# Kernel tuning notes

Measured on AMD Instinct MI355X. Metric: run time of the kernel, lower is better.

## Reference

```python
import jax, jax.numpy as jnp
import numpy as np
import math

NUM_HEADS = 8
EPS = 1e-5
LEAKY_SLOPE = 0.01


def _attention(q, k, v, mask):
    # q:[S,64] k,v:[T,64] -> [S,64]; scale by sqrt(d) per source (q.shape[1])
    s = (q @ k.T) / math.sqrt(q.shape[1])
    if mask:
        S, T = s.shape
        tri = jnp.tril(jnp.ones((S, T), dtype=bool))
        s = jnp.where(tri, s, -jnp.inf)
    return jax.nn.softmax(s, axis=1) @ v


def _mha(q, k, v, w_o, mask):
    # all heads share the same (q,k,v) in the source, so cat over heads == tile
    head = _attention(q, k, v, mask)            # [S,64]
    concat = jnp.tile(head, (1, NUM_HEADS))     # [S,512]
    return concat @ w_o


def _layernorm(x, g, b):
    mu = jnp.mean(x, axis=-1, keepdims=True)
    var = jnp.var(x, axis=-1, keepdims=True)
    return (x - mu) * jax.lax.rsqrt(var + EPS) * g + b


def setup_inputs() -> dict:
    key = jax.random.key(0)
    ks = jax.random.split(key, 12)
    S, D, P, H = 8192, 512, 64, 2048
    sd = 1.0 / math.sqrt(D)
    return {
        "encoder_output": jax.random.normal(ks[0], (S, D), jnp.float32),
        "previous_stage_output": jax.random.normal(ks[1], (S, D), jnp.float32),
        "wq_m": jax.random.normal(ks[2], (D, P), jnp.float32) * sd,
        "wk_m": jax.random.normal(ks[3], (D, P), jnp.float32) * sd,
        "wv_m": jax.random.normal(ks[4], (D, P), jnp.float32) * sd,
        "wq_c": jax.random.normal(ks[5], (D, P), jnp.float32) * sd,
        "wk_c": jax.random.normal(ks[6], (D, P), jnp.float32) * sd,
        "wv_c": jax.random.normal(ks[7], (D, P), jnp.float32) * sd,
        "w_o": jax.random.normal(ks[8], (D, D), jnp.float32) * sd,
        "ln_g": jnp.ones((D,), jnp.float32),
        "ln_b": jnp.zeros((D,), jnp.float32),
        "w1": jax.random.normal(ks[9], (D, H), jnp.float32) * sd,
        "b1": jnp.zeros((H,), jnp.float32),
        "w2": jax.random.normal(ks[10], (H, D), jnp.float32) * (1.0 / math.sqrt(H)),
        "b2": jnp.zeros((D,), jnp.float32),
    }


def reference(encoder_output, previous_stage_output, wq_m, wk_m, wv_m,
              wq_c, wk_c, wv_c, w_o, ln_g, ln_b, w1, b1, w2, b2):
    prev = previous_stage_output
    # masked (causal) self-attention over previous decoder output
    masked_mh = _mha(prev @ wq_m, prev @ wk_m, prev @ wv_m, w_o, mask=True)
    # cross attention: q from masked output, k/v from encoder output
    mh = _mha(masked_mh @ wq_c, encoder_output @ wk_c, encoder_output @ wv_c,
              w_o, mask=False)
    x = _layernorm(mh + prev, ln_g, ln_b)
    h = x @ w1 + b1
    h = jnp.where(h >= 0, h, LEAKY_SLOPE * h)
    ffn = h @ w2 + b2
    out = _layernorm(ffn + x, ln_g, ln_b)
    return (encoder_output, out)
```

## Files before the change

kernel.cpp:

```cpp
#include <hip/hip_runtime.h>
#include <hip/hip_bf16.h>

typedef unsigned short u16;
typedef __attribute__((ext_vector_type(4))) float f32x4;
typedef __attribute__((ext_vector_type(8))) __bf16 bf16x8;
typedef __attribute__((ext_vector_type(8))) short short8;
typedef __attribute__((ext_vector_type(4))) short s16x4;

constexpr int SEQ = 8192;
constexpr int DM  = 512;
constexpr int HD  = 64;
constexpr int HFF = 2048;

__device__ __forceinline__ float b2f(u16 u){
  union { unsigned int i; float f; } v; v.i = ((unsigned int)u) << 16; return v.f;
}
__device__ __forceinline__ u16 f2b(float f){
  union { float f; unsigned int i; } v; v.f = f;
  unsigned int r = v.i + 0x7FFFu + ((v.i >> 16) & 1u);
  return (u16)(r >> 16);
}

__device__ __forceinline__ void gload16(const u16* g, u16* lds){
  __builtin_amdgcn_global_load_lds(
      (const __attribute__((address_space(1))) void*)g,
      (__attribute__((address_space(3))) void*)lds, 16, 0, 0);
}

__global__ __launch_bounds__(256) void cvt2_k(const float* __restrict__ enc,
                                              const float* __restrict__ prev,
                                              float* __restrict__ outf,
                                              u16* __restrict__ enc_b,
                                              u16* __restrict__ prev_b, long n8){
  long i = blockIdx.x * 256L + threadIdx.x;
  if(i >= n8) return;
  const float* in = blockIdx.y ? prev : enc;
  u16* ob = blockIdx.y ? prev_b : enc_b;
  f32x4 a = ((const f32x4*)in)[i*2];
  f32x4 b = ((const f32x4*)in)[i*2+1];
  if(!blockIdx.y){
    ((f32x4*)outf)[i*2]   = a;
    ((f32x4*)outf)[i*2+1] = b;
  }
  u16 ov[8];
  for(int j=0;j<4;j++){ ov[j] = f2b(a[j]); ov[4+j] = f2b(b[j]); }
  ((short8*)ob)[i] = *(short8*)ov;
}

__global__ __launch_bounds__(256) void prep_k(const float* __restrict__ p0,
                                              const float* __restrict__ p1,
                                              const float* __restrict__ p2,
                                              const float* __restrict__ p3,
                                              const float* __restrict__ p4,
                                              const float* __restrict__ p5,
                                              const float* __restrict__ w1,
                                              const float* __restrict__ w2,
                                              const float* __restrict__ wo,
                                              u16* __restrict__ out6,
                                              u16* __restrict__ w1_t,
                                              u16* __restrict__ w2_t,
                                              u16* __restrict__ wost){
  __shared__ u16 t[32][33];
  const int z = blockIdx.z;
  const int tx = threadIdx.x, ty = threadIdx.y;
  if(z < 6){
    if(blockIdx.x >= 2) return;
    const float* ins[6] = {p0,p1,p2,p3,p4,p5};
    const float* in = ins[z];
    u16* o = out6 + (long)z * 32768;
    int c0 = blockIdx.x*32, r0 = blockIdx.y*32;
    for(int i=0;i<4;i++)
      t[ty+i*8][tx] = f2b(in[(long)(r0+ty+i*8)*HD + c0+tx]);
    __syncthreads();
    for(int i=0;i<4;i++) o[(long)(c0+ty+i*8)*DM + r0+tx] = t[tx][ty+i*8];
  } else if(z == 6){
    int c0 = blockIdx.x*32, r0 = blockIdx.y*32;
    for(int i=0;i<4;i++)
      t[ty+i*8][tx] = f2b(w1[(long)(r0+ty+i*8)*HFF + c0+tx]);
    __syncthreads();
    for(int i=0;i<4;i++) w1_t[(long)(c0+ty+i*8)*DM + r0+tx] = t[tx][ty+i*8];
  } else if(z == 7){
    int c0 = blockIdx.y*32, r0 = blockIdx.x*32;
    for(int i=0;i<4;i++)
      t[ty+i*8][tx] = f2b(w2[(long)(r0+ty+i*8)*DM + c0+tx]);
    __syncthreads();
    for(int i=0;i<4;i++) w2_t[(long)(c0+ty+i*8)*HFF + r0+tx] = t[tx][ty+i*8];
  } else {
    int fb = blockIdx.y*64 + blockIdx.x;
    if(fb >= 128) return;
    int tid = fb*256 + ty*32 + tx;
    int n = tid >> 6, p = tid & 63;
    float s = 0.f;
    for(int h=0; h<8; h++) s += wo[(long)(h*64+p)*DM + n];
    wost[n*64+p] = f2b(s);
  }
}

__global__ __launch_bounds__(256) void vtrans2_k(const u16* __restrict__ v0,
                                                 u16* __restrict__ o0,
                                                 const u16* __restrict__ v1,
                                                 u16* __restrict__ o1){
  __shared__ u16 t[32][33];
  const u16* in = blockIdx.z ? v1 : v0;
  u16* o = blockIdx.z ? o1 : o0;
  int c0 = blockIdx.x*32, r0 = blockIdx.y*32;
  int tx = threadIdx.x, ty = threadIdx.y;
  for(int i=0;i<4;i++) t[ty+i*8][tx] = in[(long)(r0+ty+i*8)*HD + c0+tx];
  __syncthreads();
  for(int i=0;i<4;i++) o[(long)(c0+ty+i*8)*SEQ + r0+tx] = t[tx][ty+i*8];
}

template<bool WRITE_BF>
__global__ __launch_bounds__(256) void add_ln(const u16* __restrict__ Xa,
                                              const float* __restrict__ Xb,
                                              const float* __restrict__ G,
                                              const float* __restrict__ Bb,
                                              float* __restrict__ OutF,
                                              u16* __restrict__ OutB){
  int row  = blockIdx.x*4 + (threadIdx.x>>6);
  int lane = threadIdx.x & 63;
  short8 a8 = *(const short8*)&Xa[(long)row*DM + lane*8];
  f32x4 b0 = *(const f32x4*)&Xb[(long)row*DM + lane*8];
  f32x4 b1 = *(const f32x4*)&Xb[(long)row*DM + lane*8 + 4];
  float x[8]; float s=0.f, s2=0.f;
  for(int i=0;i<8;i++){
    float bv = (i<4) ? b0[i] : b1[i-4];
    x[i] = b2f((u16)a8[i]) + bv;
    s += x[i]; s2 += x[i]*x[i];
  }
  for(int o=1;o<64;o<<=1){ s += __shfl_xor(s,o); s2 += __shfl_xor(s2,o); }
  float mu  = s * (1.f/DM);
  float var = s2 * (1.f/DM) - mu*mu;
  float rstd = rsqrtf(var + 1e-5f);
  f32x4 g0 = *(const f32x4*)&G[lane*8];
  f32x4 g1 = *(const f32x4*)&G[lane*8+4];
  f32x4 p0 = *(const f32x4*)&Bb[lane*8];
  f32x4 p1 = *(const f32x4*)&Bb[lane*8+4];
  float of[8]; u16 ob[8];
  for(int i=0;i<8;i++){
    float gv = (i<4)?g0[i]:g1[i-4], bv2 = (i<4)?p0[i]:p1[i-4];
    float v = (x[i]-mu)*rstd*gv + bv2;
    of[i] = v; ob[i] = f2b(v);
  }
  *(f32x4*)&OutF[(long)row*DM + lane*8]     = *(f32x4*)&of[0];
  *(f32x4*)&OutF[(long)row*DM + lane*8 + 4] = *(f32x4*)&of[4];
  if constexpr (WRITE_BF)
    *(short8*)&OutB[(long)row*DM + lane*8] = *(short8*)ob;
}

template<int BM,int BN,int EPI,bool DBUF>
__global__ __launch_bounds__(256) void gemm2(const u16* __restrict__ A,
                                             const u16* __restrict__ Bt,
                                             u16* __restrict__ C,
                                             const float* __restrict__ bias,
                                             int N, int K, long sB, long sC){
  constexpr int WR=2, WC=2;
  constexpr int WM = BM/WR, WN = BN/WC;
  constexpr int MF = WM/16, NF = WN/16;
  constexpr int NB = DBUF ? 2 : 1;
  __shared__ u16 As[NB][BM*64];
  __shared__ u16 Bs[NB][BN*64];

  const int tid = threadIdx.x;
  const int wid = tid >> 6, lane = tid & 63;
  const int g = lane >> 4, lr = lane & 15;
  const int m0 = blockIdx.x * BM;
  const int n0 = blockIdx.y * BN;
  Bt += (long)blockIdx.z * sB;
  C  += (long)blockIdx.z * sC;
  const int wr = wid / WC, wc = wid % WC;

  f32x4 acc[MF][NF];
  for(int m=0;m<MF;m++) for(int n=0;n<NF;n++) acc[m][n] = (f32x4)0.f;

  auto stage = [&](const u16* src, int base_row, u16* lds, int rows, int k0){
    const int cpw = rows/32;
    for(int i=0;i<cpw;i++){
      int chunk = wid*cpw + i;
      int Lb = chunk*1024;
      int L  = Lb + lane*16;
      int row = L >> 7, cb = L & 127;
      int scb = cb ^ ((row&7)<<4);
      gload16(&src[(long)(base_row+row)*K + k0 + (scb>>1)], lds + (Lb>>1));
    }
  };
  auto compute = [&](const u16* As_, const u16* Bs_){
    for(int kc=0;kc<2;kc++){
      const int co = (kc*32 + g*8) ^ ((lr&7)<<3);
      bf16x8 af[MF], bfr[NF];
      for(int m=0;m<MF;m++) af[m]  = *(const bf16x8*)&As_[(wr*WM+m*16+lr)*64 + co];
      for(int n=0;n<NF;n++) bfr[n] = *(const bf16x8*)&Bs_[(wc*WN+n*16+lr)*64 + co];
      for(int m=0;m<MF;m++)
        for(int n=0;n<NF;n++)
          acc[m][n] = __builtin_amdgcn_mfma_f32_16x16x32_bf16(af[m], bfr[n], acc[m][n], 0,0,0);
    }
  };

  const int nk = K/64;
  if constexpr (DBUF){
    stage(A, m0, As[0], BM, 0);
    stage(Bt, n0, Bs[0], BN, 0);
    __syncthreads();
    int cur = 0;
    for(int t=0;t<nk;t++){
      if(t+1<nk){
        stage(A, m0, As[cur^1], BM, (t+1)*64);
        stage(Bt, n0, Bs[cur^1], BN, (t+1)*64);
      }
      compute(As[cur], Bs[cur]);
      __syncthreads();
      cur ^= 1;
    }
  } else {
    for(int t=0;t<nk;t++){
      stage(A, m0, As[0], BM, t*64);
      stage(Bt, n0, Bs[0], BN, t*64);
      __syncthreads();
      compute(As[0], Bs[0]);
      __syncthreads();
    }
  }
  for(int m=0;m<MF;m++){
    int row = m0 + wr*WM + m*16 + g*4;
    for(int n=0;n<NF;n++){
      int col = n0 + wc*WN + n*16 + lr;
      float bv = 0.f;
      if constexpr (EPI>=1) bv = bias[col];
      for(int j=0;j<4;j++){
        float v = acc[m][n][j] + bv;
        if constexpr (EPI==2) v = (v >= 0.f) ? v : 0.01f*v;
        C[(long)(row+j)*N + col] = f2b(v);
      }
    }
  }
}

template<bool CAUSAL, int NCH>
__global__ __launch_bounds__(256) void attn_part_k(const u16* __restrict__ Q,
                                                   const u16* __restrict__ Km,
                                                   const u16* __restrict__ Vt,
                                                   u16* __restrict__ Op,
                                                   float* __restrict__ Ml){
  constexpr int LDK = 72;
  constexpr int CTI = 128/NCH;
  __shared__ u16 Ks[64*LDK];
  __shared__ u16 Vs[64*LDK];
  __shared__ u16 Ps[4*16*LDK];

  const int qb = blockIdx.x, ci = blockIdx.y;
  if(CAUSAL && ci*CTI > qb) return;

  const int tid = threadIdx.x, wid = tid>>6, lane = tid&63;
  const int g = lane>>4, lr = lane&15, r4 = g*4;
  const int qrow = qb*64 + wid*16;

  bf16x8 qf[2];
  for(int kc=0;kc<2;kc++){
    bf16x8 t = *(const bf16x8*)&Q[(long)(qrow + lr)*HD + kc*32 + g*8];
    for(int i=0;i<8;i++) t[i] = (__bf16)((float)t[i] * 0.1803368801f);
    qf[kc] = t;
  }

  f32x4 o[4]; for(int n=0;n<4;n++) o[n] = (f32x4)0.f;
  float mst = -1e30f, lst = 0.f;

  const int tdiag = qb - ci*CTI;
  const int tmax = CAUSAL ? min(CTI, tdiag + 1) : CTI;
  const int kvbase = ci*CTI*64;

  const int sr0 = tid>>3, sc0 = (tid&7)*8;
  short8 rK0, rK1, rV0, rV1;
  {
    rK0 = *(const short8*)&Km[(long)(kvbase+sr0)*HD + sc0];
    rK1 = *(const short8*)&Km[(long)(kvbase+sr0+32)*HD + sc0];
    rV0 = *(const short8*)&Vt[(long)sr0*SEQ + kvbase + sc0];
    rV1 = *(const short8*)&Vt[(long)(sr0+32)*SEQ + kvbase + sc0];
  }

  for(int t=0; t<tmax; ++t){
    const int kv0 = kvbase + t*64;
    __syncthreads();
    *(short8*)&Ks[sr0*LDK + sc0]      = rK0;
    *(short8*)&Ks[(sr0+32)*LDK + sc0] = rK1;
    *(short8*)&Vs[sr0*LDK + sc0]      = rV0;
    *(short8*)&Vs[(sr0+32)*LDK + sc0] = rV1;
    __syncthreads();
    if(t+1 < tmax){
      const int kn = kv0 + 64;
      rK0 = *(const short8*)&Km[(long)(kn+sr0)*HD + sc0];
      rK1 = *(const short8*)&Km[(long)(kn+sr0+32)*HD + sc0];
      rV0 = *(const short8*)&Vt[(long)sr0*SEQ + kn + sc0];
      rV1 = *(const short8*)&Vt[(long)(sr0+32)*SEQ + kn + sc0];
    }

    f32x4 s[4]; for(int n=0;n<4;n++) s[n] = (f32x4)0.f;
    for(int kc=0;kc<2;kc++){
      for(int n=0;n<4;n++){
        bf16x8 kf = *(const bf16x8*)&Ks[(n*16+lr)*LDK + kc*32 + g*8];
        s[n] = __builtin_amdgcn_mfma_f32_16x16x32_bf16(kf, qf[kc], s[n], 0,0,0);
      }
    }
    if(CAUSAL && t == tdiag){
      int row = qrow + lr;
      for(int n=0;n<4;n++)
        for(int j=0;j<4;j++)
          if(kv0 + n*16 + r4 + j > row) s[n][j] = -1e30f;
    }
    float m01 = fmaxf(fmaxf(s[0][0],s[0][1]), fmaxf(s[0][2],s[0][3]));
    float m11 = fmaxf(fmaxf(s[1][0],s[1][1]), fmaxf(s[1][2],s[1][3]));
    float m21 = fmaxf(fmaxf(s[2][0],s[2][1]), fmaxf(s[2][2],s[2][3]));
    float m31 = fmaxf(fmaxf(s[3][0],s[3][1]), fmaxf(s[3][2],s[3][3]));
    float pmax = fmaxf(fmaxf(m01,m11), fmaxf(m21,m31));
    pmax = fmaxf(pmax, __shfl_xor(pmax,16));
    pmax = fmaxf(pmax, __shfl_xor(pmax,32));
    if(__any(pmax > mst + 8.f)){
      float mn = fmaxf(mst, pmax);
      float fac = exp2f(mst - mn);
      mst = mn; lst *= fac;
      float fj0 = __shfl(fac, r4+0), fj1 = __shfl(fac, r4+1);
      float fj2 = __shfl(fac, r4+2), fj3 = __shfl(fac, r4+3);
      for(int n=0;n<4;n++){
        o[n][0] *= fj0; o[n][1] *= fj1; o[n][2] *= fj2; o[n][3] *= fj3;
      }
    }
    float rs = 0.f;
    for(int n=0;n<4;n++){
      u16 w[4];
      for(int j=0;j<4;j++){
        float p = exp2f(s[n][j] - mst);
        rs += p;
        __bf16 pb = (__bf16)p;
        union { __bf16 b; u16 u; } cv; cv.b = pb;
        w[j] = cv.u;
      }
      *(s16x4*)&Ps[(wid*16 + lr)*LDK + n*16 + r4] = *(s16x4*)w;
    }
    rs += __shfl_xor(rs,16); rs += __shfl_xor(rs,32);
    lst += rs;
    for(int kc=0;kc<2;kc++){
      bf16x8 pf = *(const bf16x8*)&Ps[(wid*16 + lr)*LDK + kc*32 + g*8];
      for(int n=0;n<4;n++){
        bf16x8 vf = *(const bf16x8*)&Vs[(n*16+lr)*LDK + kc*32 + g*8];
        o[n] = __builtin_amdgcn_mfma_f32_16x16x32_bf16(pf, vf, o[n], 0,0,0);
      }
    }
  }
  const long pr = (long)(qb*NCH + ci)*64;
  for(int n=0;n<4;n++)
    for(int j=0;j<4;j++)
      Op[(pr + wid*16 + r4 + j)*64 + n*16 + lr] = f2b(o[n][j]);
  if(lane < 16){
    Ml[(pr + wid*16 + lr)*2]     = mst;
    Ml[(pr + wid*16 + lr)*2 + 1] = lst;
  }
}

template<bool CAUSAL, int NCH>
__global__ __launch_bounds__(256) void attn_red_k(const u16* __restrict__ Op,
                                                  const float* __restrict__ Ml,
                                                  u16* __restrict__ O){
  constexpr int CTI = 128/NCH;
  int r = blockIdx.x*4 + (threadIdx.x>>6);
  int d = threadIdx.x & 63;
  int qb = r >> 6, rt = r & 63;
  int nch = CAUSAL ? (qb/CTI) + 1 : NCH;
  long base = (long)qb*NCH*64 + rt;
  float m = -1e30f;
  for(int i=0;i<nch;i++) m = fmaxf(m, Ml[(base + i*64)*2]);
  float L = 0.f, acc = 0.f;
  for(int i=0;i<nch;i++){
    float mi = Ml[(base + i*64)*2], li = Ml[(base + i*64)*2 + 1];
    float w = exp2f(mi - m);
    L   += li * w;
    acc += w * b2f(Op[(base + i*64)*64 + d]);
  }
  O[(long)r*HD + d] = f2b(acc / L);
}

extern "C" void kernel_launch(void* const* d_in, const int* in_sizes, int n_in,
                              void* d_out, int out_size, void* d_ws, size_t ws_size,
                              hipStream_t stream){
  const float* enc  = (const float*)d_in[0];
  const float* prev = (const float*)d_in[1];
  const float* wq_m = (const float*)d_in[2];
  const float* wk_m = (const float*)d_in[3];
  const float* wv_m = (const float*)d_in[4];
  const float* wq_c = (const float*)d_in[5];
  const float* wk_c = (const float*)d_in[6];
  const float* wv_c = (const float*)d_in[7];
  const float* w_o  = (const float*)d_in[8];
  const float* ln_g = (const float*)d_in[9];
  const float* ln_b = (const float*)d_in[10];
  const float* w1   = (const float*)d_in[11];
  const float* b1   = (const float*)d_in[12];
  const float* w2   = (const float*)d_in[13];
  const float* b2   = (const float*)d_in[14];
  float* out = (float*)d_out;
  u16* ws  = (u16*)d_ws;

  u16* wq_m_t = ws;
  u16* wk_c_t = wq_m_t + 4*32768;
  u16* wost   = wq_m_t + 6*32768;
  u16* w1_t   = wost   + 32768;
  u16* w2_t   = w1_t   + 1048576;
  u16* enc_b  = w2_t   + 1048576;
  u16* prev_b = enc_b  + 4194304;
  u16* q_m    = prev_b + 4194304;
  u16* k_m    = q_m    + 524288;
  u16* v_m    = k_m    + 524288;
  u16* v_m_t  = v_m    + 524288;
  u16* head_m = v_m_t  + 524288;
  u16* k_c    = head_m + 524288;
  u16* v_c    = k_c    + 524288;
  u16* v_c_t  = v_c    + 524288;
  u16* q_c    = v_c_t  + 524288;
  u16* head_c = q_c    + 524288;
  u16* mmh    = head_c + 524288;
  u16* mh     = mmh    + 4194304;
  u16* xb     = mh     + 4194304;
  float* xf   = (float*)(xb + 4194304);
  u16* hbuf   = enc_b;
  u16* ffn    = mh;
  u16* Op     = mmh;
  float* Ml   = (float*)(Op + (long)128*32*64*64);

  dim3 b256(256), tb(32,8);

  cvt2_k<<<dim3(2048,2), b256, 0, stream>>>(enc, prev, out, enc_b, prev_b, (long)SEQ*DM/8);

  prep_k<<<dim3(64,16,9), tb, 0, stream>>>(wq_m, wk_m, wv_m, wq_c, wk_c, wv_c,
                                           w1, w2, w_o, wq_m_t, w1_t, w2_t, wost);

  gemm2<64,64,0,true><<<dim3(SEQ/64,1,3), b256, 0, stream>>>(prev_b, wq_m_t, q_m, nullptr, HD, DM, 32768, 524288);
  gemm2<64,64,0,true><<<dim3(SEQ/64,1,2), b256, 0, stream>>>(enc_b,  wk_c_t, k_c, nullptr, HD, DM, 32768, 524288);
  vtrans2_k<<<dim3(2,256,2), tb, 0, stream>>>(v_m, v_m_t, v_c, v_c_t);

  attn_part_k<true,32><<<dim3(SEQ/64, 32), b256, 0, stream>>>(q_m, k_m, v_m_t, Op, Ml);
  attn_red_k<true,32><<<dim3(SEQ/4), b256, 0, stream>>>(Op, Ml, head_m);
  gemm2<64,128,0,false><<<dim3(SEQ/64,4,1), b256, 0, stream>>>(head_m, wost, mmh, nullptr, DM, HD, 0, 0);

  gemm2<64,64,0,false><<<dim3(SEQ/64,1,1), b256, 0, stream>>>(mmh, wq_m_t + 3*32768, q_c, nullptr, HD, DM, 0, 0);
  attn_part_k<false,16><<<dim3(SEQ/64, 16), b256, 0, stream>>>(q_c, k_c, v_c_t, Op, Ml);
  attn_red_k<false,16><<<dim3(SEQ/4), b256, 0, stream>>>(Op, Ml, head_c);
  gemm2<64,128,0,false><<<dim3(SEQ/64,4,1), b256, 0, stream>>>(head_c, wost, mh, nullptr, DM, HD, 0, 0);

  add_ln<true><<<dim3(SEQ/4), b256, 0, stream>>>(mh, prev, ln_g, ln_b, xf, xb);

  gemm2<128,128,2,false><<<dim3(SEQ/128,HFF/128,1), b256, 0, stream>>>(xb, w1_t, hbuf, b1, HFF, DM, 0, 0);
  gemm2<64,128,1,false><<<dim3(SEQ/64,4,1),         b256, 0, stream>>>(hbuf, w2_t, ffn, b2, DM, HFF, 0, 0);

  add_ln<false><<<dim3(SEQ/4), b256, 0, stream>>>(ffn, xf, ln_g, ln_b, out + (long)SEQ*DM, nullptr);
}
```

Baseline: 227.6 us.

## Widen attention blocks to 128 query rows sharing each K/V tile

The attention partial kernel now uses 512-thread blocks covering 128 query rows (eight waves), so each staged 64-row K/V tile in LDS is reused by twice as many query waves. The causal version drops from 32 to 16 KV chunks, with per-wave iteration limits so waves in the upper half skip tiles beyond their diagonal while still joining the block barriers. The aim is to halve K/V global loads and staging per query row and to give the reduction kernel fewer partials to combine. In exchange there are fewer, larger blocks, idle waves in causal diagonal tiles, and longer per-block chains in the causal pass.

```diff
diff --git a/kernel.cpp b/kernel.cpp
--- a/kernel.cpp
+++ b/kernel.cpp
@@ -235,24 +235,27 @@
   }
 }
 
-template<bool CAUSAL, int NCH>
-__global__ __launch_bounds__(256) void attn_part_k(const u16* __restrict__ Q,
+template<bool CAUSAL>
+__global__ __launch_bounds__(512) void attn_part_k(const u16* __restrict__ Q,
                                                    const u16* __restrict__ Km,
                                                    const u16* __restrict__ Vt,
                                                    u16* __restrict__ Op,
                                                    float* __restrict__ Ml){
   constexpr int LDK = 72;
-  constexpr int CTI = 128/NCH;
+  constexpr int NCH = 16;
+  constexpr int CTI = 8;
   __shared__ u16 Ks[64*LDK];
   __shared__ u16 Vs[64*LDK];
-  __shared__ u16 Ps[4*16*LDK];
+  __shared__ u16 Ps[8*16*LDK];
 
   const int qb = blockIdx.x, ci = blockIdx.y;
-  if(CAUSAL && ci*CTI > qb) return;
+  const int tdiag_b = 2*qb + 1 - ci*CTI;
+  if(CAUSAL && tdiag_b < 0) return;
 
   const int tid = threadIdx.x, wid = tid>>6, lane = tid&63;
   const int g = lane>>4, lr = lane&15, r4 = g*4;
-  const int qrow = qb*64 + wid*16;
+  const int qrow = qb*128 + wid*16;
+  const int qb64 = qrow>>6;
 
   bf16x8 qf[2];
   for(int kc=0;kc<2;kc++){
@@ -264,94 +267,89 @@
   f32x4 o[4]; for(int n=0;n<4;n++) o[n] = (f32x4)0.f;
   float mst = -1e30f, lst = 0.f;
 
-  const int tdiag = qb - ci*CTI;
-  const int tmax = CAUSAL ? min(CTI, tdiag + 1) : CTI;
-  const int kvbase = ci*CTI*64;
+  const int tdiag_w = CAUSAL ? (qb64 - ci*CTI) : 0;
+  const int tmax_w  = CAUSAL ? min(CTI, tdiag_w + 1) : CTI;
+  const int tmax_b  = CAUSAL ? min(CTI, tdiag_b + 1) : CTI;
+  const int kvbase  = ci*CTI*64;
 
   const int sr0 = tid>>3, sc0 = (tid&7)*8;
-  short8 rK0, rK1, rV0, rV1;
-  {
-    rK0 = *(const short8*)&Km[(long)(kvbase+sr0)*HD + sc0];
-    rK1 = *(const short8*)&Km[(long)(kvbase+sr0+32)*HD + sc0];
-    rV0 = *(const short8*)&Vt[(long)sr0*SEQ + kvbase + sc0];
-    rV1 = *(const short8*)&Vt[(long)(sr0+32)*SEQ + kvbase + sc0];
-  }
-
-  for(int t=0; t<tmax; ++t){
+  short8 rK, rV;
+  rK = *(const short8*)&Km[(long)(kvbase+sr0)*HD + sc0];
+  rV = *(const short8*)&Vt[(long)sr0*SEQ + kvbase + sc0];
+
+  for(int t=0; t<tmax_b; ++t){
     const int kv0 = kvbase + t*64;
     __syncthreads();
-    *(short8*)&Ks[sr0*LDK + sc0]      = rK0;
-    *(short8*)&Ks[(sr0+32)*LDK + sc0] = rK1;
-    *(short8*)&Vs[sr0*LDK + sc0]      = rV0;
-    *(short8*)&Vs[(sr0+32)*LDK + sc0] = rV1;
-    __syncthreads();
-    if(t+1 < tmax){
+    *(short8*)&Ks[sr0*LDK + sc0] = rK;
+    *(short8*)&Vs[sr0*LDK + sc0] = rV;
+    __syncthreads();
+    if(t+1 < tmax_b){
       const int kn = kv0 + 64;
-      rK0 = *(const short8*)&Km[(long)(kn+sr0)*HD + sc0];
-      rK1 = *(const short8*)&Km[(long)(kn+sr0+32)*HD + sc0];
-      rV0 = *(const short8*)&Vt[(long)sr0*SEQ + kn + sc0];
-      rV1 = *(const short8*)&Vt[(long)(sr0+32)*SEQ + kn + sc0];
-    }
-
-    f32x4 s[4]; for(int n=0;n<4;n++) s[n] = (f32x4)0.f;
-    for(int kc=0;kc<2;kc++){
+      rK = *(const short8*)&Km[(long)(kn+sr0)*HD + sc0];
+      rV = *(const short8*)&Vt[(long)sr0*SEQ + kn + sc0];
+    }
+    if(t < tmax_w){
+      f32x4 s[4]; for(int n=0;n<4;n++) s[n] = (f32x4)0.f;
+      for(int kc=0;kc<2;kc++){
+        for(int n=0;n<4;n++){
+          bf16x8 kf = *(const bf16x8*)&Ks[(n*16+lr)*LDK + kc*32 + g*8];
+          s[n] = __builtin_amdgcn_mfma_f32_16x16x32_bf16(kf, qf[kc], s[n], 0,0,0);
+        }
+      }
+      if(CAUSAL && t == tdiag_w){
+        int row = qrow + lr;
+        for(int n=0;n<4;n++)
+          for(int j=0;j<4;j++)
+            if(kv0 + n*16 + r4 + j > row) s[n][j] = -1e30f;
+      }
+      float m01 = fmaxf(fmaxf(s[0][0],s[0][1]), fmaxf(s[0][2],s[0][3]));
+      float m11 = fmaxf(fmaxf(s[1][0],s[1][1]), fmaxf(s[1][2],s[1][3]));
+      float m21 = fmaxf(fmaxf(s[2][0],s[2][1]), fmaxf(s[2][2],s[2][3]));
+      float m31 = fmaxf(fmaxf(s[3][0],s[3][1]), fmaxf(s[3][2],s[3][3]));
+      float pmax = fmaxf(fmaxf(m01,m11), fmaxf(m21,m31));
+      pmax = fmaxf(pmax, __shfl_xor(pmax,16));
+      pmax = fmaxf(pmax, __shfl_xor(pmax,32));
+      if(__any(pmax > mst + 8.f)){
+        float mn = fmaxf(mst, pmax);
+        float fac = exp2f(mst - mn);
+        mst = mn; lst *= fac;
+        float fj0 = __shfl(fac, r4+0), fj1 = __shfl(fac, r4+1);
+        float fj2 = __shfl(fac, r4+2), fj3 = __shfl(fac, r4+3);
+        for(int n=0;n<4;n++){
+          o[n][0] *= fj0; o[n][1] *= fj1; o[n][2] *= fj2; o[n][3] *= fj3;
+        }
+      }
+      float rs = 0.f;
       for(int n=0;n<4;n++){
-        bf16x8 kf = *(const bf16x8*)&Ks[(n*16+lr)*LDK + kc*32 + g*8];
-        s[n] = __builtin_amdgcn_mfma_f32_16x16x32_bf16(kf, qf[kc], s[n], 0,0,0);
-      }
-    }
-    if(CAUSAL && t == tdiag){
-      int row = qrow + lr;
-      for(int n=0;n<4;n++)
-        for(int j=0;j<4;j++)
-          if(kv0 + n*16 + r4 + j > row) s[n][j] = -1e30f;
-    }
-    float m01 = fmaxf(fmaxf(s[0][0],s[0][1]), fmaxf(s[0][2],s[0][3]));
-    float m11 = fmaxf(fmaxf(s[1][0],s[1][1]), fmaxf(s[1][2],s[1][3]));
-    float m21 = fmaxf(fmaxf(s[2][0],s[2][1]), fmaxf(s[2][2],s[2][3]));
-    float m31 = fmaxf(fmaxf(s[3][0],s[3][1]), fmaxf(s[3][2],s[3][3]));
-    float pmax = fmaxf(fmaxf(m01,m11), fmaxf(m21,m31));
-    pmax = fmaxf(pmax, __shfl_xor(pmax,16));
-    pmax = fmaxf(pmax, __shfl_xor(pmax,32));
-    if(__any(pmax > mst + 8.f)){
-      float mn = fmaxf(mst, pmax);
-      float fac = exp2f(mst - mn);
-      mst = mn; lst *= fac;
-      float fj0 = __shfl(fac, r4+0), fj1 = __shfl(fac, r4+1);
-      float fj2 = __shfl(fac, r4+2), fj3 = __shfl(fac, r4+3);
-      for(int n=0;n<4;n++){
-        o[n][0] *= fj0; o[n][1] *= fj1; o[n][2] *= fj2; o[n][3] *= fj3;
-      }
-    }
-    float rs = 0.f;
-    for(int n=0;n<4;n++){
-      u16 w[4];
-      for(int j=0;j<4;j++){
-        float p = exp2f(s[n][j] - mst);
-        rs += p;
-        __bf16 pb = (__bf16)p;
-        union { __bf16 b; u16 u; } cv; cv.b = pb;
-        w[j] = cv.u;
-      }
-      *(s16x4*)&Ps[(wid*16 + lr)*LDK + n*16 + r4] = *(s16x4*)w;
-    }
-    rs += __shfl_xor(rs,16); rs += __shfl_xor(rs,32);
-    lst += rs;
-    for(int kc=0;kc<2;kc++){
-      bf16x8 pf = *(const bf16x8*)&Ps[(wid*16 + lr)*LDK + kc*32 + g*8];
-      for(int n=0;n<4;n++){
-        bf16x8 vf = *(const bf16x8*)&Vs[(n*16+lr)*LDK + kc*32 + g*8];
-        o[n] = __builtin_amdgcn_mfma_f32_16x16x32_bf16(pf, vf, o[n], 0,0,0);
-      }
-    }
-  }
-  const long pr = (long)(qb*NCH + ci)*64;
+        u16 w[4];
+        for(int j=0;j<4;j++){
+          float p = exp2f(s[n][j] - mst);
+          rs += p;
+          __bf16 pb = (__bf16)p;
+          union { __bf16 b; u16 u; } cv; cv.b = pb;
+          w[j] = cv.u;
+        }
+        *(s16x4*)&Ps[(wid*16 + lr)*LDK + n*16 + r4] = *(s16x4*)w;
+      }
+      rs += __shfl_xor(rs,16); rs += __shfl_xor(rs,32);
+      lst += rs;
+      for(int kc=0;kc<2;kc++){
+        bf16x8 pf = *(const bf16x8*)&Ps[(wid*16 + lr)*LDK + kc*32 + g*8];
+        for(int n=0;n<4;n++){
+          bf16x8 vf = *(const bf16x8*)&Vs[(n*16+lr)*LDK + kc*32 + g*8];
+          o[n] = __builtin_amdgcn_mfma_f32_16x16x32_bf16(pf, vf, o[n], 0,0,0);
+        }
+      }
+    }
+  }
+  const long pr = (long)(qb64*NCH + ci)*64;
+  const int ro = (wid&3)*16;
   for(int n=0;n<4;n++)
     for(int j=0;j<4;j++)
-      Op[(pr + wid*16 + r4 + j)*64 + n*16 + lr] = f2b(o[n][j]);
+      Op[(pr + ro + r4 + j)*64 + n*16 + lr] = f2b(o[n][j]);
   if(lane < 16){
-    Ml[(pr + wid*16 + lr)*2]     = mst;
-    Ml[(pr + wid*16 + lr)*2 + 1] = lst;
+    Ml[(pr + ro + lr)*2]     = mst;
+    Ml[(pr + ro + lr)*2 + 1] = lst;
   }
 }
 
@@ -422,9 +420,9 @@
   u16* hbuf   = enc_b;
   u16* ffn    = mh;
   u16* Op     = mmh;
-  float* Ml   = (float*)(Op + (long)128*32*64*64);
-
-  dim3 b256(256), tb(32,8);
+  float* Ml   = (float*)(Op + (long)128*16*64*64);
+
+  dim3 b256(256), b512(512), tb(32,8);
 
   cvt2_k<<<dim3(2048,2), b256, 0, stream>>>(enc, prev, out, enc_b, prev_b, (long)SEQ*DM/8);
 
@@ -435,12 +433,12 @@
   gemm2<64,64,0,true><<<dim3(SEQ/64,1,2), b256, 0, stream>>>(enc_b,  wk_c_t, k_c, nullptr, HD, DM, 32768, 524288);
   vtrans2_k<<<dim3(2,256,2), tb, 0, stream>>>(v_m, v_m_t, v_c, v_c_t);
 
-  attn_part_k<true,32><<<dim3(SEQ/64, 32), b256, 0, stream>>>(q_m, k_m, v_m_t, Op, Ml);
-  attn_red_k<true,32><<<dim3(SEQ/4), b256, 0, stream>>>(Op, Ml, head_m);
+  attn_part_k<true><<<dim3(SEQ/128, 16), b512, 0, stream>>>(q_m, k_m, v_m_t, Op, Ml);
+  attn_red_k<true,16><<<dim3(SEQ/4), b256, 0, stream>>>(Op, Ml, head_m);
   gemm2<64,128,0,false><<<dim3(SEQ/64,4,1), b256, 0, stream>>>(head_m, wost, mmh, nullptr, DM, HD, 0, 0);
 
   gemm2<64,64,0,false><<<dim3(SEQ/64,1,1), b256, 0, stream>>>(mmh, wq_m_t + 3*32768, q_c, nullptr, HD, DM, 0, 0);
-  attn_part_k<false,16><<<dim3(SEQ/64, 16), b256, 0, stream>>>(q_c, k_c, v_c_t, Op, Ml);
+  attn_part_k<false><<<dim3(SEQ/128, 16), b512, 0, stream>>>(q_c, k_c, v_c_t, Op, Ml);
   attn_red_k<false,16><<<dim3(SEQ/4), b256, 0, stream>>>(Op, Ml, head_c);
   gemm2<64,128,0,false><<<dim3(SEQ/64,4,1), b256, 0, stream>>>(head_c, wost, mh, nullptr, DM, HD, 0, 0);
 
```

After: 224.7 us. About the same (-1.3%).
